# Optimization experiments

Hardware: AMD Instinct MI355X
Metric: run time of the kernel (lower is better)

Reference implementation:

```python
import jax, jax.numpy as jnp
import numpy as np

# Model constants (match init_kwargs config)
D_MODEL, D_INNER, D_HEAD, N_HEADS = 1024, 2048, 64, 32
D_STATE, D_CONV, CHUNK, N_LAYERS = 64, 4, 256, 2
CONV_DIM = D_INNER + 2 * D_STATE        # n_groups = 1
D_IN_PROJ = 2 * D_INNER + 2 * D_STATE + N_HEADS
B_SZ, L_SEQ = 2, 4096
EPS = 1e-5


def setup_inputs() -> dict:
    key = jax.random.key(0)
    ks = jax.random.split(key, 8)
    x = jax.random.normal(ks[0], (B_SZ, L_SEQ, D_MODEL), jnp.float32)
    in_proj_w = jax.random.normal(ks[1], (N_LAYERS, D_IN_PROJ, D_MODEL), jnp.float32) * 0.02
    conv_w = jax.random.normal(ks[2], (N_LAYERS, CONV_DIM, D_CONV), jnp.float32) * 0.2
    conv_b = jax.random.normal(ks[3], (N_LAYERS, CONV_DIM), jnp.float32) * 0.02
    # dt_bias init as in the torch code: inverse-softplus of dt ~ LogUniform(1e-3, 1e-1)
    dt = jnp.exp(jax.random.uniform(ks[4], (N_LAYERS, N_HEADS))
                 * (np.log(0.1) - np.log(0.001)) + np.log(0.001))
    dt = jnp.clip(dt, 1e-4, None)
    dt_bias = dt + jnp.log(-jnp.expm1(-dt))
    A_log = jnp.log(jax.random.uniform(ks[5], (N_LAYERS, N_HEADS), minval=1.0, maxval=16.0))
    D = jnp.ones((N_LAYERS, N_HEADS), jnp.float32)
    gnorm_w = jnp.ones((N_LAYERS, D_INNER), jnp.float32)
    out_proj_w = jax.random.normal(ks[6], (N_LAYERS, D_MODEL, D_INNER), jnp.float32) * 0.02
    norm_w = jnp.ones((N_LAYERS, D_MODEL), jnp.float32)
    return dict(x=x, in_proj_w=in_proj_w, conv_w=conv_w, conv_b=conv_b, dt_bias=dt_bias,
                A_log=A_log, D=D, gnorm_w=gnorm_w, out_proj_w=out_proj_w, norm_w=norm_w)


def _rmsnorm(x, w, eps=EPS):
    return x * jax.lax.rsqrt(jnp.mean(x * x, axis=-1, keepdims=True) + eps) * w


def _segsum(x):
    # x: (..., T) -> (..., T, T) with S[i, j] = sum_{j < k <= i} x[k], -inf above diag
    T = x.shape[-1]
    cs = jnp.cumsum(x, axis=-1)
    d = cs[..., :, None] - cs[..., None, :]
    return jnp.where(jnp.tril(jnp.ones((T, T), bool)), d, -jnp.inf)


def _causal_conv1d(x, w, b):
    # depthwise causal conv: x (B,L,C), w (C,K), b (C)
    K = w.shape[-1]
    L = x.shape[1]
    xp = jnp.pad(x, ((0, 0), (K - 1, 0), (0, 0)))
    out = jnp.broadcast_to(b, x.shape)
    for i in range(K):
        out = out + xp[:, i:i + L, :] * w[:, i]
    return out


def _ssd(X, dt, A, B, C, D):
    # Exact chunked SSD scan (mamba_chunk_scan_combined), n_groups=1.
    # X (b,l,h,p), dt (b,l,h), A (h), B,C (b,l,n)
    b, l, h, p = X.shape
    n = B.shape[-1]
    nc = l // CHUNK
    Xdt = X * dt[..., None]
    dA = (dt * A).reshape(b, nc, CHUNK, h).transpose(0, 3, 1, 2)     # (b,h,z,c)
    dAcs = jnp.cumsum(dA, axis=-1)
    Lmat = jnp.exp(_segsum(dA))                                      # (b,h,z,c,c)
    Bc = B.reshape(b, nc, CHUNK, n)
    Cc = C.reshape(b, nc, CHUNK, n)
    Xc = Xdt.reshape(b, nc, CHUNK, h, p)
    # intra-chunk (diagonal) part
    G = jnp.einsum('bzln,bzsn->bzls', Cc, Bc)                        # (b,z,c,c)
    M = G[:, None] * Lmat                                            # (b,h,z,c,c)
    Yd = jnp.einsum('bhzls,bzshp->bzlhp', M, Xc)
    # chunk states
    decay_states = jnp.exp(dAcs[..., -1:] - dAcs)                    # (b,h,z,c)
    states = jnp.einsum('bzln,bhzl,bzlhp->bzhpn', Bc, decay_states, Xc)
    # inter-chunk recurrence
    chunk_decay = jnp.exp(_segsum(jnp.pad(dAcs[..., -1], ((0, 0), (0, 0), (1, 0)))))
    states0 = jnp.concatenate([jnp.zeros_like(states[:, :1]), states], axis=1)
    prev = jnp.einsum('bhzc,bchpn->bzhpn', chunk_decay, states0)[:, :-1]
    Yo = jnp.einsum('bzln,bzhpn,bhzl->bzlhp', Cc, prev, jnp.exp(dAcs))
    Y = (Yd + Yo).reshape(b, l, h, p) + X * D[None, None, :, None]
    return Y


def _block(x, in_w, cw, cb, dtb, a_log, d_skip, gw, ow, nw):
    b, l, _ = x.shape
    h = _rmsnorm(x, nw)
    zxbcdt = jnp.einsum('bld,ed->ble', h, in_w)
    z = zxbcdt[..., :D_INNER]
    xBC = zxbcdt[..., D_INNER:D_INNER + CONV_DIM]
    dt = jax.nn.softplus(zxbcdt[..., D_INNER + CONV_DIM:] + dtb)      # (b,l,H)
    xBC = jax.nn.silu(_causal_conv1d(xBC, cw, cb))
    xs = xBC[..., :D_INNER].reshape(b, l, N_HEADS, D_HEAD)
    Bm = xBC[..., D_INNER:D_INNER + D_STATE]
    Cm = xBC[..., D_INNER + D_STATE:]
    A = -jnp.exp(a_log)
    y = _ssd(xs, dt, A, Bm, Cm, d_skip).reshape(b, l, D_INNER)
    y = _rmsnorm(y * jax.nn.silu(z), gw)                              # gated RMSNorm (gate before norm)
    return x + jnp.einsum('bli,di->bld', y, ow)


def reference(x, in_proj_w, conv_w, conv_b, dt_bias, A_log, D, gnorm_w, out_proj_w, norm_w):
    for i in range(in_proj_w.shape[0]):
        x = _block(x, in_proj_w[i], conv_w[i], conv_b[i], dt_bias[i],
                   A_log[i], D[i], gnorm_w[i], out_proj_w[i], norm_w[i])
    return x
```

## Files before the change

### kernel.cpp

```cpp
#include <hip/hip_runtime.h>

#define DMODEL   1024
#define DINNER   2048
#define NHEADS   32
#define DHEAD    64
#define DSTATE   64
#define CONVDIM  2176
#define DINPROJ  4256
#define LSEQ     4096
#define BSZ      2
#define NCHUNK   16
#define CHUNK    256
#define NROWS    8192
#define NPAD     4352
#define XT_P     264

typedef __attribute__((ext_vector_type(8))) short  short8;
typedef __attribute__((ext_vector_type(4))) float  f32x4;
typedef __attribute__((ext_vector_type(4))) unsigned short us4;

__device__ __forceinline__ float bf2f(unsigned short u){
  return __uint_as_float(((unsigned int)u) << 16);
}
__device__ __forceinline__ unsigned short f2bf(float f){
  unsigned int i = __float_as_uint(f);
  i += 0x7fffu + ((i >> 16) & 1u);
  return (unsigned short)(i >> 16);
}

__device__ __forceinline__ void gl_lds16(const void* g, void* l){
  __builtin_amdgcn_global_load_lds(
      (const __attribute__((address_space(1))) unsigned int*)g,
      (__attribute__((address_space(3))) unsigned int*)l, 16, 0, 0);
}

__global__ void cast_pad_kernel(const float* __restrict__ src, unsigned short* __restrict__ dst,
                                int rows_src, int cols, long long total){
  long long i = (long long)blockIdx.x * 256 + threadIdx.x;
  if (i >= total) return;
  long long r = i / cols;
  dst[i] = (r < rows_src) ? f2bf(src[i]) : (unsigned short)0;
}

__global__ void rmsnorm_kernel(const float* __restrict__ x, const float* __restrict__ w,
                               unsigned short* __restrict__ out){
  int r = blockIdx.x, t = threadIdx.x;
  const float* xr = x + (size_t)r * DMODEL;
  float v[4]; float s = 0.f;
#pragma unroll
  for (int i = 0; i < 4; ++i){ v[i] = xr[t + i*256]; s += v[i]*v[i]; }
  __shared__ float red[4];
  for (int off = 32; off; off >>= 1) s += __shfl_down(s, off, 64);
  if ((t & 63) == 0) red[t >> 6] = s;
  __syncthreads();
  s = red[0] + red[1] + red[2] + red[3];
  float sc = rsqrtf(s * (1.f/DMODEL) + 1e-5f);
#pragma unroll
  for (int i = 0; i < 4; ++i)
    out[(size_t)r*DMODEL + t + i*256] = f2bf(v[i]*sc*w[t + i*256]);
}

template<int EPI>
__launch_bounds__(256, 3)
__global__ void gemm_bt(const unsigned short* __restrict__ A, const unsigned short* __restrict__ Bw,
                        void* __restrict__ Cout, const float* __restrict__ Cres,
                        int K, int Nstore){
  __shared__ __align__(16) unsigned short As[128*64];
  __shared__ __align__(16) unsigned short Bs[128*64];
  const int m0 = blockIdx.y * 128, n0 = blockIdx.x * 128;
  const int t = threadIdx.x, w = t >> 6, lane = t & 63;
  const int wr = w >> 1, wc = w & 1;
  const int srow = lane >> 3;
  const int scol = (lane & 7) * 8;
  f32x4 acc[4][4] = {};

  for (int k0 = 0; k0 < K; k0 += 64){
#pragma unroll
    for (int it = 0; it < 4; ++it){
      int rr = (w*4 + it)*8 + srow;
      gl_lds16(A  + (size_t)(m0 + rr)*K + k0 + scol, &As[(w*4 + it)*512]);
      gl_lds16(Bw + (size_t)(n0 + rr)*K + k0 + scol, &Bs[(w*4 + it)*512]);
    }
    __syncthreads();
#pragma unroll
    for (int kk = 0; kk < 64; kk += 32){
      short8 af[4], bfr[4];
      int col = kk + (lane >> 4)*8;
#pragma unroll
      for (int m = 0; m < 4; ++m)
        af[m] = *(const short8*)&As[(wr*64 + m*16 + (lane & 15))*64 + col];
#pragma unroll
      for (int n = 0; n < 4; ++n)
        bfr[n] = *(const short8*)&Bs[(wc*64 + n*16 + (lane & 15))*64 + col];
#pragma unroll
      for (int m = 0; m < 4; ++m)
#pragma unroll
        for (int n = 0; n < 4; ++n)
          acc[m][n] = __builtin_amdgcn_mfma_f32_16x16x32_bf16(af[m], bfr[n], acc[m][n], 0, 0, 0);
    }
    __syncthreads();
  }

#pragma unroll
  for (int m = 0; m < 4; ++m){
#pragma unroll
    for (int n = 0; n < 4; ++n){
      int col = n0 + wc*64 + n*16 + (lane & 15);
      if (col < Nstore){
#pragma unroll
        for (int r = 0; r < 4; ++r){
          int row = m0 + wr*64 + m*16 + (lane >> 4)*4 + r;
          if (EPI == 0)
            ((unsigned short*)Cout)[(size_t)row*Nstore + col] = f2bf(acc[m][n][r]);
          else
            ((float*)Cout)[(size_t)row*Nstore + col] =
                Cres[(size_t)row*Nstore + col] + acc[m][n][r];
        }
      }
    }
  }
}

__global__ void conv_silu_kernel(const unsigned short* __restrict__ zx,
                                 const float* __restrict__ cw, const float* __restrict__ cb,
                                 unsigned short* __restrict__ X, unsigned short* __restrict__ Bm,
                                 unsigned short* __restrict__ Cm){
  int gid = blockIdx.x*256 + threadIdx.x;
  if (gid >= (CONVDIM/8)*(NROWS/64)) return;
  const int oc = gid % (CONVDIM/8);
  const int rb = gid / (CONVDIM/8);
  const int c = oc*8;
  const size_t r0 = (size_t)rb*64;
  const int l0 = (int)(r0 & (LSEQ-1));
  float w[4][8], bias[8];
#pragma unroll
  for (int j = 0; j < 8; ++j){
    bias[j] = cb[c+j];
#pragma unroll
    for (int i = 0; i < 4; ++i) w[i][j] = cw[(c+j)*4 + i];
  }
  const unsigned short* src = zx + DINNER + c;
  float p[3][8];
#pragma unroll
  for (int i = 0; i < 3; ++i){
    if (l0 - 3 + i >= 0){
      short8 v = *(const short8*)(src + (r0 - 3 + i)*DINPROJ);
#pragma unroll
      for (int j = 0; j < 8; ++j) p[i][j] = bf2f((unsigned short)v[j]);
    } else {
#pragma unroll
      for (int j = 0; j < 8; ++j) p[i][j] = 0.f;
    }
  }
  for (int it = 0; it < 64; ++it){
    const size_t r = r0 + it;
    short8 v = *(const short8*)(src + r*DINPROJ);
    float cur[8];
    short8 ov;
#pragma unroll
    for (int j = 0; j < 8; ++j){
      cur[j] = bf2f((unsigned short)v[j]);
      float a = bias[j] + w[0][j]*p[0][j] + w[1][j]*p[1][j] + w[2][j]*p[2][j] + w[3][j]*cur[j];
      float s = a / (1.f + __expf(-a));
      ov[j] = (short)f2bf(s);
    }
    if (c < DINNER)             *(short8*)(X  + r*DINNER + c) = ov;
    else if (c < DINNER+DSTATE) *(short8*)(Bm + r*DSTATE + (c-DINNER)) = ov;
    else                        *(short8*)(Cm + r*DSTATE + (c-DINNER-DSTATE)) = ov;
#pragma unroll
    for (int j = 0; j < 8; ++j){ p[0][j]=p[1][j]; p[1][j]=p[2][j]; p[2][j]=cur[j]; }
  }
}

__global__ void dtscan_kernel(const unsigned short* __restrict__ zx, const float* __restrict__ dtb,
                              const float* __restrict__ A_log,
                              float* __restrict__ dt_sp, float* __restrict__ dAcs_g){
  const int z = blockIdx.x, hh = blockIdx.y, b = blockIdx.z;
  const int t = threadIdx.x;
  __shared__ float sdA[CHUNK];
  const float Ah = -__expf(A_log[hh]);
  size_t r = (size_t)b*LSEQ + z*CHUNK + t;
  float raw = bf2f(zx[r*DINPROJ + DINNER + CONVDIM + hh]) + dtb[hh];
  float dtv = raw > 20.f ? raw : log1pf(__expf(raw));
  sdA[t] = dtv * Ah;
  __syncthreads();
  for (int off = 1; off < CHUNK; off <<= 1){
    float v = (t >= off) ? sdA[t - off] : 0.f;
    __syncthreads();
    sdA[t] += v;
    __syncthreads();
  }
  size_t hb = (size_t)(b*NHEADS + hh);
  dt_sp[hb*LSEQ + z*CHUNK + t] = dtv;
  dAcs_g[(hb*NCHUNK + z)*CHUNK + t] = sdA[t];
}

__launch_bounds__(256, 4)
__global__ void gram_kernel(const unsigned short* __restrict__ Bm,
                            const unsigned short* __restrict__ Cm,
                            unsigned short* __restrict__ Gb){
  const int zq = blockIdx.x, b = blockIdx.y;
  const int z = zq >> 2, rq = zq & 3;
  const int t = threadIdx.x, w = t >> 6, lane = t & 63;
  const size_t row0 = (size_t)b*LSEQ + z*CHUNK;
  f32x4 acc[4][4] = {};
#pragma unroll
  for (int k2 = 0; k2 < 2; ++k2){
    int kc = k2*32 + (lane >> 4)*8;
    short8 cf[4], bfr[4];
#pragma unroll
    for (int mf = 0; mf < 4; ++mf)
      cf[mf] = *(const short8*)(Cm + (row0 + rq*64 + mf*16 + (lane & 15))*DSTATE + kc);
#pragma unroll
    for (int nf = 0; nf < 4; ++nf)
      bfr[nf] = *(const short8*)(Bm + (row0 + w*64 + nf*16 + (lane & 15))*DSTATE + kc);
#pragma unroll
    for (int mf = 0; mf < 4; ++mf)
#pragma unroll
      for (int nf = 0; nf < 4; ++nf)
        acc[mf][nf] = __builtin_amdgcn_mfma_f32_16x16x32_bf16(cf[mf], bfr[nf], acc[mf][nf], 0, 0, 0);
  }
  unsigned short* Gp = Gb + (((size_t)b*NCHUNK + z) << 16);
#pragma unroll
  for (int mf = 0; mf < 4; ++mf)
#pragma unroll
    for (int nf = 0; nf < 4; ++nf)
#pragma unroll
      for (int r = 0; r < 4; ++r){
        int row = rq*64 + mf*16 + (lane >> 4)*4 + r;
        int col = w*64 + nf*16 + (lane & 15);
        Gp[(size_t)row*256 + col] = f2bf(acc[mf][nf][r]);
      }
}

__launch_bounds__(256, 2)
__global__ void chunk_main_kernel(const unsigned short* __restrict__ X,
                                  const unsigned short* __restrict__ Bm,
                                  const unsigned short* __restrict__ Gb,
                                  const float* __restrict__ dt_sp,
                                  const float* __restrict__ dAcs_g,
                                  float* __restrict__ states,
                                  unsigned short* __restrict__ Yb){
  const int z = blockIdx.x, hh = blockIdx.y, b = blockIdx.z;
  const int t = threadIdx.x, w = t >> 6, lane = t & 63;
  __shared__ __align__(16) unsigned short Xt[64 * XT_P];
  __shared__ __align__(16) unsigned short U[64 * XT_P];
  __shared__ float sdA[CHUNK];
  __shared__ float sdt[CHUNK];

  const size_t row0 = (size_t)b*LSEQ + z*CHUNK;
  const size_t hb = (size_t)(b*NHEADS + hh);
  sdA[t] = dAcs_g[(hb*NCHUNK + z)*CHUNK + t];
  sdt[t] = dt_sp[hb*LSEQ + z*CHUNK + t];
  __syncthreads();
  const float total = sdA[CHUNK-1];

  for (int it = 0; it < 16; ++it){
    int l = it*16 + (t >> 4);
    int p4 = (t & 15) * 4;
    float dtl = sdt[l];
    float dec = __expf(total - sdA[l]);
    us4 xv = *(const us4*)(X  + (row0 + l)*DINNER + hh*DHEAD + p4);
    us4 bv = *(const us4*)(Bm + (row0 + l)*DSTATE + p4);
#pragma unroll
    for (int j = 0; j < 4; ++j){
      Xt[(p4 + j)*XT_P + l] = f2bf(bf2f(xv[j]) * dtl);
      U [(p4 + j)*XT_P + l] = f2bf(bf2f(bv[j]) * dec);
    }
  }
  __syncthreads();

  {
    f32x4 sacc[4] = {};
    for (int k2 = 0; k2 < 8; ++k2){
      int kc = k2*32 + (lane >> 4)*8;
      short8 a = *(const short8*)&U[(w*16 + (lane & 15))*XT_P + kc];
#pragma unroll
      for (int pt = 0; pt < 4; ++pt){
        short8 bfr = *(const short8*)&Xt[(pt*16 + (lane & 15))*XT_P + kc];
        sacc[pt] = __builtin_amdgcn_mfma_f32_16x16x32_bf16(a, bfr, sacc[pt], 0, 0, 0);
      }
    }
    float* sp = states + (((size_t)b*NCHUNK + z)*NHEADS + hh)*(DHEAD*DSTATE);
#pragma unroll
    for (int pt = 0; pt < 4; ++pt){
      int p = pt*16 + (lane & 15);
#pragma unroll
      for (int r = 0; r < 4; ++r){
        int n = w*16 + (lane >> 4)*4 + r;
        sp[p*DSTATE + n] = sacc[pt][r];
      }
    }
  }
  __syncthreads();

  const unsigned short* Gp = Gb + (((size_t)b*NCHUNK + z) << 16);
  f32x4 yacc[4][4] = {};
  for (int st = 0; st < 8; ++st){
    short8 xb[4];
#pragma unroll
    for (int pt = 0; pt < 4; ++pt)
      xb[pt] = *(const short8*)&Xt[(pt*16 + (lane & 15))*XT_P + st*32 + (lane >> 4)*8];
    const int s0 = st*32 + (lane >> 4)*8;
    float es[8];
#pragma unroll
    for (int j = 0; j < 8; ++j) es[j] = sdA[s0 + j];
#pragma unroll
    for (int lt = 0; lt < 4; ++lt){
      int lg = w + lt*4;
      if (st*32 > lg*16 + 15) continue;
      int l = lg*16 + (lane & 15);
      float el = sdA[l];
      short8 gv = *(const short8*)&Gp[(size_t)l*256 + s0];
      short8 mf;
#pragma unroll
      for (int j = 0; j < 8; ++j){
        float m = (s0 + j <= l) ? bf2f((unsigned short)gv[j]) * __expf(el - es[j]) : 0.f;
        mf[j] = (short)f2bf(m);
      }
#pragma unroll
      for (int pt = 0; pt < 4; ++pt)
        yacc[lt][pt] = __builtin_amdgcn_mfma_f32_16x16x32_bf16(mf, xb[pt], yacc[lt][pt], 0, 0, 0);
    }
  }
  __syncthreads();

  unsigned short* Yst = U + w * 4096;
#pragma unroll
  for (int lt = 0; lt < 4; ++lt)
#pragma unroll
    for (int pt = 0; pt < 4; ++pt)
#pragma unroll
      for (int r = 0; r < 4; ++r){
        int row = lt*16 + (lane >> 4)*4 + r;
        int c = pt*16 + (lane & 15);
        int cs = (c & 7) | ((((c >> 3) ^ (row & 7)) & 7) << 3);
        Yst[row*64 + cs] = f2bf(yacc[lt][pt][r]);
      }
  __syncthreads();
  {
    int ltl = lane >> 4, rr = lane & 15;
    int row = ltl*16 + rr;
    int lg = (w + ltl*4)*16 + rr;
    unsigned short* dst = Yb + (row0 + lg)*DINNER + hh*DHEAD;
#pragma unroll
    for (int k = 0; k < 8; ++k){
      short8 v = *(const short8*)&Yst[row*64 + ((k ^ (row & 7)) << 3)];
      *(short8*)(dst + k*8) = v;
    }
  }
}

__launch_bounds__(256)
__global__ void state_recur_kernel(const float* __restrict__ states, const float* __restrict__ dAcs_g,
                                   unsigned short* __restrict__ prev_bf){
  const int hh = blockIdx.x, b = blockIdx.y, t = threadIdx.x;
  float S[16];
#pragma unroll
  for (int k = 0; k < 16; ++k) S[k] = 0.f;
  for (int z = 0; z < NCHUNK; ++z){
    size_t base = (((size_t)b*NCHUNK + z)*NHEADS + hh)*(DHEAD*DSTATE);
    float cd = __expf(dAcs_g[(((size_t)(b*NHEADS + hh))*NCHUNK + z)*CHUNK + CHUNK-1]);
#pragma unroll
    for (int k = 0; k < 16; ++k){
      size_t idx = base + (size_t)k*256 + t;
      float st = states[idx];
      prev_bf[idx] = f2bf(S[k]);
      S[k] = S[k]*cd + st;
    }
  }
}

__launch_bounds__(512, 2)
__global__ void chunk_fin_kernel(const unsigned short* __restrict__ X,
                                 const unsigned short* __restrict__ Cm,
                                 const unsigned short* __restrict__ zx,
                                 const float* __restrict__ dAcs_g,
                                 const unsigned short* __restrict__ prev_bf,
                                 const float* __restrict__ Dp,
                                 const unsigned short* __restrict__ Yb,
                                 const float* __restrict__ gnw,
                                 unsigned short* __restrict__ yn){
  const int s = blockIdx.x;
  const int b = blockIdx.y;
  const int z = s >> 4, sl = s & 15;
  const int t = threadIdx.x, w = t >> 6, lane = t & 63;
  const size_t row0 = (size_t)b*LSEQ + z*CHUNK + sl*16;
  __shared__ __align__(16) unsigned short Yg[16][2056];
  __shared__ float seA[NHEADS][16];
  __shared__ float sDp[NHEADS];

  {
    int hh = t >> 4, r = t & 15;
    seA[hh][r] = __expf(dAcs_g[(((size_t)(b*NHEADS + hh))*NCHUNK + z)*CHUNK + sl*16 + r]);
    if (t < NHEADS) sDp[t] = Dp[t];
  }
  __syncthreads();

  short8 cf[2];
#pragma unroll
  for (int k2 = 0; k2 < 2; ++k2)
    cf[k2] = *(const short8*)(Cm + (row0 + (lane & 15))*DSTATE + k2*32 + (lane >> 4)*8);

  for (int hi = 0; hi < 4; ++hi){
    int hh = w*4 + hi;
    const unsigned short* pvb = prev_bf + (((size_t)b*NCHUNK + z)*NHEADS + hh)*(DHEAD*DSTATE);
    f32x4 acc[4] = {};
#pragma unroll
    for (int k2 = 0; k2 < 2; ++k2){
      int kc = k2*32 + (lane >> 4)*8;
#pragma unroll
      for (int pt = 0; pt < 4; ++pt){
        short8 bv = *(const short8*)(pvb + (size_t)(pt*16 + (lane & 15))*DSTATE + kc);
        acc[pt] = __builtin_amdgcn_mfma_f32_16x16x32_bf16(cf[k2], bv, acc[pt], 0, 0, 0);
      }
    }
#pragma unroll
    for (int pt = 0; pt < 4; ++pt){
      int c = hh*DHEAD + pt*16 + (lane & 15);
#pragma unroll
      for (int r = 0; r < 4; ++r){
        int row = (lane >> 4)*4 + r;
        Yg[row][c] = f2bf(acc[pt][r] * seA[hh][row]);
      }
    }
  }
  __syncthreads();

  const int row = t >> 5, i = t & 31;
  const size_t grow = row0 + row;
  float ss = 0.f;
#pragma unroll
  for (int j = 0; j < 8; ++j){
    int c0 = i*8 + j*256;
    short8 yo = *(const short8*)&Yg[row][c0];
    short8 yd = *(const short8*)(Yb + grow*DINNER + c0);
    short8 xv = *(const short8*)(X  + grow*DINNER + c0);
    short8 zv = *(const short8*)(zx + grow*DINPROJ + c0);
    float Dh = sDp[c0 >> 6];
    short8 og;
#pragma unroll
    for (int q = 0; q < 8; ++q){
      float y = bf2f((unsigned short)yd[q]) + bf2f((unsigned short)yo[q])
              + Dh*bf2f((unsigned short)xv[q]);
      float zf = bf2f((unsigned short)zv[q]);
      float g = y * (zf / (1.f + __expf(-zf)));
      ss += g*g;
      og[q] = (short)f2bf(g);
    }
    *(short8*)&Yg[row][c0] = og;
  }
  for (int off = 16; off; off >>= 1) ss += __shfl_down(ss, off, 32);
  float sc = __shfl(ss, 0, 32);
  sc = rsqrtf(sc * (1.f/DINNER) + 1e-5f);
  __syncthreads();

#pragma unroll
  for (int j = 0; j < 8; ++j){
    int c0 = i*8 + j*256;
    short8 g = *(const short8*)&Yg[row][c0];
    f32x4 w0 = *(const f32x4*)(gnw + c0);
    f32x4 w1 = *(const f32x4*)(gnw + c0 + 4);
    short8 o;
#pragma unroll
    for (int q = 0; q < 4; ++q) o[q]   = (short)f2bf(bf2f((unsigned short)g[q])  *sc*w0[q]);
#pragma unroll
    for (int q = 0; q < 4; ++q) o[q+4] = (short)f2bf(bf2f((unsigned short)g[q+4])*sc*w1[q]);
    *(short8*)(yn + grow*DINNER + c0) = o;
  }
}

extern "C" void kernel_launch(void* const* d_in, const int* in_sizes, int n_in,
                              void* d_out, int out_size, void* d_ws, size_t ws_size,
                              hipStream_t stream){
  const float* x      = (const float*)d_in[0];
  const float* in_w   = (const float*)d_in[1];
  const float* conv_w = (const float*)d_in[2];
  const float* conv_b = (const float*)d_in[3];
  const float* dt_b   = (const float*)d_in[4];
  const float* A_log  = (const float*)d_in[5];
  const float* Dp     = (const float*)d_in[6];
  const float* gnw    = (const float*)d_in[7];
  const float* out_w  = (const float*)d_in[8];
  const float* norm_w = (const float*)d_in[9];
  float* outp = (float*)d_out;

  const size_t NEEDED =
      (size_t)NROWS*DMODEL*2 + (size_t)NPAD*DMODEL*2 + (size_t)DMODEL*DINNER*2
    + (size_t)NROWS*DINPROJ*2 + (size_t)NROWS*DINNER*2  + (size_t)NROWS*DINNER*2
    + (size_t)NROWS*DSTATE*2*2 + (size_t)BSZ*NHEADS*LSEQ*4
    + (size_t)BSZ*NHEADS*NCHUNK*CHUNK*4
    + (size_t)BSZ*NCHUNK*NHEADS*DHEAD*DSTATE*4
    + (size_t)BSZ*NCHUNK*NHEADS*DHEAD*DSTATE*2
    + (size_t)BSZ*NCHUNK*CHUNK*CHUNK*2
    + 48*256;
  if (ws_size < NEEDED) return;

  char* p = (char*)d_ws;
  auto alloc = [&](size_t n){ char* r = p; p += (n + 255) & ~(size_t)255; return (void*)r; };
  unsigned short* h    = (unsigned short*)alloc((size_t)NROWS*DMODEL*2);
  unsigned short* wA   = (unsigned short*)alloc((size_t)NPAD*DMODEL*2);
  unsigned short* wO   = (unsigned short*)alloc((size_t)DMODEL*DINNER*2);
  unsigned short* zx   = (unsigned short*)alloc((size_t)NROWS*DINPROJ*2);
  unsigned short* X    = (unsigned short*)alloc((size_t)NROWS*DINNER*2);
  unsigned short* Yb   = (unsigned short*)alloc((size_t)NROWS*DINNER*2);
  unsigned short* Bm   = (unsigned short*)alloc((size_t)NROWS*DSTATE*2);
  unsigned short* Cm   = (unsigned short*)alloc((size_t)NROWS*DSTATE*2);
  float* dtbuf  = (float*)alloc((size_t)BSZ*NHEADS*LSEQ*4);
  float* dAcs   = (float*)alloc((size_t)BSZ*NHEADS*NCHUNK*CHUNK*4);
  float* states = (float*)alloc((size_t)BSZ*NCHUNK*NHEADS*DHEAD*DSTATE*4);
  unsigned short* prev_bf = (unsigned short*)alloc((size_t)BSZ*NCHUNK*NHEADS*DHEAD*DSTATE*2);
  unsigned short* Gb = (unsigned short*)alloc((size_t)BSZ*NCHUNK*CHUNK*CHUNK*2);
  unsigned short* yn = X;

  for (int layer = 0; layer < 2; ++layer){
    const float* xprev = (layer == 0) ? x : outp;
    float* xnext = outp;

    cast_pad_kernel<<<(NPAD*DMODEL + 255)/256, 256, 0, stream>>>(
        in_w + (size_t)layer*DINPROJ*DMODEL, wA, DINPROJ, DMODEL, (long long)NPAD*DMODEL);
    rmsnorm_kernel<<<NROWS, 256, 0, stream>>>(xprev, norm_w + layer*DMODEL, h);
    gemm_bt<0><<<dim3(NPAD/128, NROWS/128), 256, 0, stream>>>(
        h, wA, (void*)zx, nullptr, DMODEL, DINPROJ);
    conv_silu_kernel<<<((CONVDIM/8)*(NROWS/64) + 255)/256, 256, 0, stream>>>(
        zx, conv_w + (size_t)layer*CONVDIM*4, conv_b + layer*CONVDIM, X, Bm, Cm);
    dtscan_kernel<<<dim3(NCHUNK, NHEADS, BSZ), 256, 0, stream>>>(
        zx, dt_b + layer*NHEADS, A_log + layer*NHEADS, dtbuf, dAcs);
    gram_kernel<<<dim3(NCHUNK*4, BSZ), 256, 0, stream>>>(Bm, Cm, Gb);
    chunk_main_kernel<<<dim3(NCHUNK, NHEADS, BSZ), 256, 0, stream>>>(
        X, Bm, Gb, dtbuf, dAcs, states, Yb);
    state_recur_kernel<<<dim3(NHEADS, BSZ), 256, 0, stream>>>(states, dAcs, prev_bf);
    chunk_fin_kernel<<<dim3(256, BSZ), 512, 0, stream>>>(
        X, Cm, zx, dAcs, prev_bf, Dp + layer*NHEADS, Yb, gnw + (size_t)layer*DINNER, yn);
    cast_pad_kernel<<<(DMODEL*DINNER + 255)/256, 256, 0, stream>>>(
        out_w + (size_t)layer*DMODEL*DINNER, wO, DMODEL, DINNER, (long long)DMODEL*DINNER);
    gemm_bt<1><<<dim3(DMODEL/128, NROWS/128), 256, 0, stream>>>(
        yn, wO, (void*)xnext, xprev, DINNER, DMODEL);
  }
  (void)in_sizes; (void)n_in; (void)out_size;
}
```

Before: 683.2 us.

## Merge weight casts into one launch and streamline small kernels

All four weight casts (both layers, in and out projections) now run in a single kernel at the start instead of four per-layer launches. rmsnorm becomes one wavefront per row with vectorized loads and stores and no shared-memory reduction. The dt scan uses wavefront shuffles instead of a barrier-heavy LDS scan, and state_recur is split four ways across blocks for more parallelism. The cost is a doubled workspace for the weight buffers.

```diff
diff --git a/kernel.cpp b/kernel.cpp
--- a/kernel.cpp
+++ b/kernel.cpp
@@ -34,30 +34,48 @@
       (__attribute__((address_space(3))) unsigned int*)l, 16, 0, 0);
 }
 
-__global__ void cast_pad_kernel(const float* __restrict__ src, unsigned short* __restrict__ dst,
-                                int rows_src, int cols, long long total){
-  long long i = (long long)blockIdx.x * 256 + threadIdx.x;
-  if (i >= total) return;
-  long long r = i / cols;
-  dst[i] = (r < rows_src) ? f2bf(src[i]) : (unsigned short)0;
-}
-
+__global__ void cast_all_kernel(const float* __restrict__ in_w, const float* __restrict__ out_w,
+                                unsigned short* __restrict__ wA, unsigned short* __restrict__ wO){
+  const long long nA = (long long)2*NPAD*DMODEL;
+  const long long nO = (long long)2*DMODEL*DINNER;
+  long long i = (long long)blockIdx.x*256 + threadIdx.x;
+  if (i < nA){
+    long long layer = i / ((long long)NPAD*DMODEL);
+    long long j = i - layer*((long long)NPAD*DMODEL);
+    long long r = j / DMODEL;
+    wA[i] = (r < DINPROJ)
+        ? f2bf(in_w[layer*((long long)DINPROJ*DMODEL) + r*DMODEL + (j - r*DMODEL)])
+        : (unsigned short)0;
+  } else if (i < nA + nO){
+    long long k = i - nA;
+    wO[k] = f2bf(out_w[k]);
+  }
+}
+
+__launch_bounds__(256)
 __global__ void rmsnorm_kernel(const float* __restrict__ x, const float* __restrict__ w,
                                unsigned short* __restrict__ out){
-  int r = blockIdx.x, t = threadIdx.x;
-  const float* xr = x + (size_t)r * DMODEL;
-  float v[4]; float s = 0.f;
-#pragma unroll
-  for (int i = 0; i < 4; ++i){ v[i] = xr[t + i*256]; s += v[i]*v[i]; }
-  __shared__ float red[4];
+  const int r = blockIdx.x*4 + (threadIdx.x >> 6);
+  const int lane = threadIdx.x & 63;
+  const float* xr = x + (size_t)r*DMODEL;
+  f32x4 v[4]; float s = 0.f;
+#pragma unroll
+  for (int i = 0; i < 4; ++i){
+    v[i] = *(const f32x4*)(xr + lane*4 + i*256);
+#pragma unroll
+    for (int j = 0; j < 4; ++j) s += v[i][j]*v[i][j];
+  }
   for (int off = 32; off; off >>= 1) s += __shfl_down(s, off, 64);
-  if ((t & 63) == 0) red[t >> 6] = s;
-  __syncthreads();
-  s = red[0] + red[1] + red[2] + red[3];
-  float sc = rsqrtf(s * (1.f/DMODEL) + 1e-5f);
-#pragma unroll
-  for (int i = 0; i < 4; ++i)
-    out[(size_t)r*DMODEL + t + i*256] = f2bf(v[i]*sc*w[t + i*256]);
+  s = __shfl(s, 0, 64);
+  const float sc = rsqrtf(s*(1.f/DMODEL) + 1e-5f);
+#pragma unroll
+  for (int i = 0; i < 4; ++i){
+    us4 o;
+    const float* wp = w + lane*4 + i*256;
+#pragma unroll
+    for (int j = 0; j < 4; ++j) o[j] = f2bf(v[i][j]*sc*wp[j]);
+    *(us4*)(out + (size_t)r*DMODEL + lane*4 + i*256) = o;
+  }
 }
 
 template<int EPI>
@@ -176,23 +194,27 @@
                               const float* __restrict__ A_log,
                               float* __restrict__ dt_sp, float* __restrict__ dAcs_g){
   const int z = blockIdx.x, hh = blockIdx.y, b = blockIdx.z;
-  const int t = threadIdx.x;
-  __shared__ float sdA[CHUNK];
+  const int t = threadIdx.x, w = t >> 6, lane = t & 63;
+  __shared__ float wsum[4];
   const float Ah = -__expf(A_log[hh]);
   size_t r = (size_t)b*LSEQ + z*CHUNK + t;
   float raw = bf2f(zx[r*DINPROJ + DINNER + CONVDIM + hh]) + dtb[hh];
   float dtv = raw > 20.f ? raw : log1pf(__expf(raw));
-  sdA[t] = dtv * Ah;
-  __syncthreads();
-  for (int off = 1; off < CHUNK; off <<= 1){
-    float v = (t >= off) ? sdA[t - off] : 0.f;
-    __syncthreads();
-    sdA[t] += v;
-    __syncthreads();
-  }
+  float v = dtv * Ah;
+#pragma unroll
+  for (int off = 1; off < 64; off <<= 1){
+    float u = __shfl_up(v, off, 64);
+    if (lane >= off) v += u;
+  }
+  if (lane == 63) wsum[w] = v;
+  __syncthreads();
+  float pre = 0.f;
+#pragma unroll
+  for (int j = 0; j < 3; ++j) if (j < w) pre += wsum[j];
+  v += pre;
   size_t hb = (size_t)(b*NHEADS + hh);
   dt_sp[hb*LSEQ + z*CHUNK + t] = dtv;
-  dAcs_g[(hb*NCHUNK + z)*CHUNK + t] = sdA[t];
+  dAcs_g[(hb*NCHUNK + z)*CHUNK + t] = v;
 }
 
 __launch_bounds__(256, 4)
@@ -354,15 +376,16 @@
 __launch_bounds__(256)
 __global__ void state_recur_kernel(const float* __restrict__ states, const float* __restrict__ dAcs_g,
                                    unsigned short* __restrict__ prev_bf){
-  const int hh = blockIdx.x, b = blockIdx.y, t = threadIdx.x;
-  float S[16];
-#pragma unroll
-  for (int k = 0; k < 16; ++k) S[k] = 0.f;
+  const int hh = blockIdx.x, b = blockIdx.y, q = blockIdx.z;
+  const int t = threadIdx.x;
+  float S[4];
+#pragma unroll
+  for (int k = 0; k < 4; ++k) S[k] = 0.f;
   for (int z = 0; z < NCHUNK; ++z){
-    size_t base = (((size_t)b*NCHUNK + z)*NHEADS + hh)*(DHEAD*DSTATE);
+    size_t base = (((size_t)b*NCHUNK + z)*NHEADS + hh)*(DHEAD*DSTATE) + (size_t)q*1024;
     float cd = __expf(dAcs_g[(((size_t)(b*NHEADS + hh))*NCHUNK + z)*CHUNK + CHUNK-1]);
 #pragma unroll
-    for (int k = 0; k < 16; ++k){
+    for (int k = 0; k < 4; ++k){
       size_t idx = base + (size_t)k*256 + t;
       float st = states[idx];
       prev_bf[idx] = f2bf(S[k]);
@@ -486,7 +509,8 @@
   float* outp = (float*)d_out;
 
   const size_t NEEDED =
-      (size_t)NROWS*DMODEL*2 + (size_t)NPAD*DMODEL*2 + (size_t)DMODEL*DINNER*2
+      (size_t)NROWS*DMODEL*2
+    + (size_t)2*NPAD*DMODEL*2 + (size_t)2*DMODEL*DINNER*2
     + (size_t)NROWS*DINPROJ*2 + (size_t)NROWS*DINNER*2  + (size_t)NROWS*DINNER*2
     + (size_t)NROWS*DSTATE*2*2 + (size_t)BSZ*NHEADS*LSEQ*4
     + (size_t)BSZ*NHEADS*NCHUNK*CHUNK*4
@@ -499,8 +523,8 @@
   char* p = (char*)d_ws;
   auto alloc = [&](size_t n){ char* r = p; p += (n + 255) & ~(size_t)255; return (void*)r; };
   unsigned short* h    = (unsigned short*)alloc((size_t)NROWS*DMODEL*2);
-  unsigned short* wA   = (unsigned short*)alloc((size_t)NPAD*DMODEL*2);
-  unsigned short* wO   = (unsigned short*)alloc((size_t)DMODEL*DINNER*2);
+  unsigned short* wA   = (unsigned short*)alloc((size_t)2*NPAD*DMODEL*2);
+  unsigned short* wO   = (unsigned short*)alloc((size_t)2*DMODEL*DINNER*2);
   unsigned short* zx   = (unsigned short*)alloc((size_t)NROWS*DINPROJ*2);
   unsigned short* X    = (unsigned short*)alloc((size_t)NROWS*DINNER*2);
   unsigned short* Yb   = (unsigned short*)alloc((size_t)NROWS*DINNER*2);
@@ -513,15 +537,20 @@
   unsigned short* Gb = (unsigned short*)alloc((size_t)BSZ*NCHUNK*CHUNK*CHUNK*2);
   unsigned short* yn = X;
 
+  {
+    long long total = (long long)2*NPAD*DMODEL + (long long)2*DMODEL*DINNER;
+    cast_all_kernel<<<(int)((total + 255)/256), 256, 0, stream>>>(in_w, out_w, wA, wO);
+  }
+
   for (int layer = 0; layer < 2; ++layer){
     const float* xprev = (layer == 0) ? x : outp;
     float* xnext = outp;
-
-    cast_pad_kernel<<<(NPAD*DMODEL + 255)/256, 256, 0, stream>>>(
-        in_w + (size_t)layer*DINPROJ*DMODEL, wA, DINPROJ, DMODEL, (long long)NPAD*DMODEL);
-    rmsnorm_kernel<<<NROWS, 256, 0, stream>>>(xprev, norm_w + layer*DMODEL, h);
+    const unsigned short* wAl = wA + (size_t)layer*NPAD*DMODEL;
+    const unsigned short* wOl = wO + (size_t)layer*DMODEL*DINNER;
+
+    rmsnorm_kernel<<<NROWS/4, 256, 0, stream>>>(xprev, norm_w + layer*DMODEL, h);
     gemm_bt<0><<<dim3(NPAD/128, NROWS/128), 256, 0, stream>>>(
-        h, wA, (void*)zx, nullptr, DMODEL, DINPROJ);
+        h, wAl, (void*)zx, nullptr, DMODEL, DINPROJ);
     conv_silu_kernel<<<((CONVDIM/8)*(NROWS/64) + 255)/256, 256, 0, stream>>>(
         zx, conv_w + (size_t)layer*CONVDIM*4, conv_b + layer*CONVDIM, X, Bm, Cm);
     dtscan_kernel<<<dim3(NCHUNK, NHEADS, BSZ), 256, 0, stream>>>(
@@ -529,13 +558,11 @@
     gram_kernel<<<dim3(NCHUNK*4, BSZ), 256, 0, stream>>>(Bm, Cm, Gb);
     chunk_main_kernel<<<dim3(NCHUNK, NHEADS, BSZ), 256, 0, stream>>>(
         X, Bm, Gb, dtbuf, dAcs, states, Yb);
-    state_recur_kernel<<<dim3(NHEADS, BSZ), 256, 0, stream>>>(states, dAcs, prev_bf);
+    state_recur_kernel<<<dim3(NHEADS, BSZ, 4), 256, 0, stream>>>(states, dAcs, prev_bf);
     chunk_fin_kernel<<<dim3(256, BSZ), 512, 0, stream>>>(
         X, Cm, zx, dAcs, prev_bf, Dp + layer*NHEADS, Yb, gnw + (size_t)layer*DINNER, yn);
-    cast_pad_kernel<<<(DMODEL*DINNER + 255)/256, 256, 0, stream>>>(
-        out_w + (size_t)layer*DMODEL*DINNER, wO, DMODEL, DINNER, (long long)DMODEL*DINNER);
     gemm_bt<1><<<dim3(DMODEL/128, NROWS/128), 256, 0, stream>>>(
-        yn, wO, (void*)xnext, xprev, DINNER, DMODEL);
+        yn, wOl, (void*)xnext, xprev, DINNER, DMODEL);
   }
   (void)in_sizes; (void)n_in; (void)out_size;
 }
```

Measured after the change: 677.8 us. About the same (-0.8%).
